# Performance work log

Measured on AMD Instinct MI355X. Metric: run time of the kernel, lower is better.

The kernel has to match this reference:

```python
import jax, jax.numpy as jnp
import numpy as np

N = 100000            # number of nodes
E = 1600000           # number of edges (avg degree 16)
D = 32                # embedding dim
MASK_DEPTH = 3        # cfg.mask_depth
PATH_PROB = 0.5       # cfg.path_prob
NUM_MASK_CAND = 1024  # cfg.num_mask_cand
EPS_NORM = 1e-12      # F.normalize eps


def setup_inputs() -> dict:
    key = jax.random.key(0)
    k1, k2 = jax.random.split(key)
    edge_index = jax.random.randint(k1, (2, E), 0, N)  # [2, E] (row, col) COO indices
    adj_values = jnp.ones((E,), dtype=jnp.float32)     # sparse values (binary adjacency)
    embeds = jax.random.normal(k2, (N, D), dtype=jnp.float32)
    return {"edge_index": edge_index, "adj_values": adj_values, "embeds": embeds}


def _spmm(rows, cols, vals, x):
    # out[i] = sum_{e: rows[e]==i} vals[e] * x[cols[e]]  -- irregular gather + scatter-add
    return jax.ops.segment_sum(x[cols] * vals[:, None], rows, num_segments=N)


def _l2_normalize(x):
    n = jnp.sqrt(jnp.sum(x * x, axis=-1, keepdims=True))
    return x / jnp.maximum(n, EPS_NORM)


def reference(edge_index, adj_values, embeds):
    rows, cols = edge_index[0], edge_index[1]
    vals = adj_values

    # order = row-sums of sparse adj, shape [N, 1]
    order = jax.ops.segment_sum(vals, rows, num_segments=N)[:, None]

    fst_emb = _spmm(rows, cols, vals, embeds) - embeds
    fst_num = order
    emb = [fst_emb]
    num = [fst_num]

    drop_key = jax.random.key(42)
    for i in range(MASK_DEPTH):
        # sparse_dropout with keep prob path_prob**(i+1); zeroing values == dropping edges in spmm
        keep_prob = PATH_PROB ** (i + 1)
        u = jax.random.uniform(jax.random.fold_in(drop_key, i), (E,))
        keep = jnp.floor(u + keep_prob)  # 1.0 with prob keep_prob, else 0.0
        vals = vals * keep               # dropout compounds across iterations

        emb.append(_spmm(rows, cols, vals, emb[-1]) - emb[-1] - order * emb[-1])
        num.append(_spmm(rows, cols, vals, num[-1]) - num[-1] - order)
        order = jax.ops.segment_sum(vals, rows, num_segments=N)[:, None]

    subgraph_embeds = sum(emb) / (sum(num) + 1e-8)
    subgraph_embeds = _l2_normalize(subgraph_embeds)
    embeds_n = _l2_normalize(embeds)

    scores = jnp.sum(subgraph_embeds * embeds_n, axis=-1)  # [N]
    # Gumbel noise: -log(-log(U))
    u = jax.random.uniform(jax.random.key(7), (N,))
    scores = scores + (-jnp.log(-jnp.log(u)))

    _, candidates = jax.lax.top_k(scores, NUM_MASK_CAND)
    return scores, candidates
```

## Files before the change

### kernel.cpp

```cpp
#include <hip/hip_runtime.h>
#include <stdint.h>
#include <stddef.h>

#define NN 100000
#define NE 1600000
#define DD 32
#define NCAND 1024
#define HSIZE 65536
#define SORTN 4096
#define NBUK ((NN + 255) / 256)
#define EPB 4096
#define BCAP 5120
#define BCAPL 4608

#define CAP1 832000
#define CAP2 432000
#define CAP3 240000

__host__ __device__ inline void tf2x32(uint32_t k0, uint32_t k1, uint32_t x0, uint32_t x1,
                                       uint32_t& o0, uint32_t& o1) {
  uint32_t ks2 = k0 ^ k1 ^ 0x1BD11BDAu;
  uint32_t v0 = x0 + k0, v1 = x1 + k1;
#define TFR(r) { v0 += v1; v1 = (v1 << (r)) | (v1 >> (32 - (r))); v1 ^= v0; }
  TFR(13) TFR(15) TFR(26) TFR(6)   v0 += k1;  v1 += ks2 + 1u;
  TFR(17) TFR(29) TFR(16) TFR(24)  v0 += ks2; v1 += k0 + 2u;
  TFR(13) TFR(15) TFR(26) TFR(6)   v0 += k0;  v1 += k1 + 3u;
  TFR(17) TFR(29) TFR(16) TFR(24)  v0 += k1;  v1 += ks2 + 4u;
  TFR(13) TFR(15) TFR(26) TFR(6)   v0 += ks2; v1 += k0 + 5u;
#undef TFR
  o0 = v0; o1 = v1;
}

__device__ __forceinline__ uint32_t jax_bits32(uint32_t k0, uint32_t k1, uint32_t i) {
  uint32_t o0, o1;
  tf2x32(k0, k1, 0u, i, o0, o1);
  return o0 ^ o1;
}

__device__ __forceinline__ float bits_to_uniform(uint32_t b) {
  return __fsub_rn(__uint_as_float((b >> 9) | 0x3f800000u), 1.0f);
}

__device__ __forceinline__ float pairwise32(const float* x) {
  float r[8];
#pragma unroll
  for (int j = 0; j < 8; ++j) r[j] = x[j];
#pragma unroll
  for (int b = 8; b < 32; b += 8)
#pragma unroll
    for (int j = 0; j < 8; ++j) r[j] = __fadd_rn(r[j], x[b + j]);
  float a01 = __fadd_rn(r[0], r[1]), a23 = __fadd_rn(r[2], r[3]);
  float a45 = __fadd_rn(r[4], r[5]), a67 = __fadd_rn(r[6], r[7]);
  return __fadd_rn(__fadd_rn(a01, a23), __fadd_rn(a45, a67));
}


__global__ __launch_bounds__(512) void kA2_bin(
    const int* __restrict__ rows, const int* __restrict__ cols,
    const float* __restrict__ adj,
    uint32_t k00, uint32_t k01, uint32_t k10, uint32_t k11,
    uint32_t k20, uint32_t k21,
    int* __restrict__ bucketCursor, int4* __restrict__ pkBin,
    int* __restrict__ bucketCntS) {
  __shared__ int hist[NBUK];
  __shared__ int base[NBUK];
  __shared__ int h1[NBUK];
  __shared__ int h2[NBUK];
  __shared__ int h3[NBUK];
  __shared__ uint8_t lvs[EPB];
  __shared__ uint16_t rank16[EPB];
  int tid = threadIdx.x;
  for (int i = tid; i < NBUK; i += 512) { hist[i] = 0; h1[i] = 0; h2[i] = 0; h3[i] = 0; }
  __syncthreads();
  int e0 = blockIdx.x * EPB;
  for (int k = 0; k < 8; ++k) {
    int e = e0 + k * 512 + tid;
    int lv = 0;
    if (e < NE) {
      float u0 = bits_to_uniform(jax_bits32(k00, k01, (uint32_t)e));
      float u1 = bits_to_uniform(jax_bits32(k10, k11, (uint32_t)e));
      float u2 = bits_to_uniform(jax_bits32(k20, k21, (uint32_t)e));
      float kp0 = floorf(__fadd_rn(u0, 0.5f));
      float kp1 = floorf(__fadd_rn(u1, 0.25f));
      float kp2 = floorf(__fadd_rn(u2, 0.125f));
      if (kp0 != 0.0f) { lv = 1; if (kp1 != 0.0f) { lv = 2; if (kp2 != 0.0f) lv = 3; } }
      int b = rows[e] >> 8;
      rank16[k * 512 + tid] = (uint16_t)atomicAdd(&hist[b], 1);
      if (lv >= 1) {
        atomicAdd(&h1[b], 1);
        if (lv >= 2) {
          atomicAdd(&h2[b], 1);
          if (lv >= 3) atomicAdd(&h3[b], 1);
        }
      }
    }
    lvs[k * 512 + tid] = (uint8_t)lv;
  }
  __syncthreads();
  for (int i = tid; i < NBUK; i += 512) {
    int h = hist[i];
    base[i] = (h > 0) ? atomicAdd(&bucketCursor[i], h) : 0;
    if (h) atomicAdd(&bucketCntS[i], h);
    if (h1[i]) atomicAdd(&bucketCntS[NBUK + i], h1[i]);
    if (h2[i]) atomicAdd(&bucketCntS[2 * NBUK + i], h2[i]);
    if (h3[i]) atomicAdd(&bucketCntS[3 * NBUK + i], h3[i]);
  }
  __syncthreads();
  for (int k = 0; k < 8; ++k) {
    int e = e0 + k * 512 + tid;
    if (e < NE) {
      int r = rows[e];
      int b = r >> 8;
      int lv = (int)lvs[k * 512 + tid];
      int pos = base[b] + (int)rank16[k * 512 + tid];
      if (pos < BCAP)
        pkBin[(size_t)b * BCAP + pos] =
            make_int4(cols[e], __float_as_int(adj[e]), (e << 2) | lv, r);
    }
  }
}

__global__ __launch_bounds__(512) void k_scanBS(const int* __restrict__ bucketCntS,
                                                int* __restrict__ bucketBaseS) {
  __shared__ int sb[512];
  int a = blockIdx.x;
  const int* c = bucketCntS + (size_t)a * NBUK;
  int* o = bucketBaseS + (size_t)a * (NBUK + 1);
  int tid = threadIdx.x;
  int v = (tid < NBUK) ? c[tid] : 0;
  sb[tid] = v;
  __syncthreads();
  for (int off = 1; off < 512; off <<= 1) {
    int x = (tid >= off) ? sb[tid - off] : 0;
    __syncthreads();
    sb[tid] += x;
    __syncthreads();
  }
  if (tid < NBUK) o[tid] = sb[tid] - v;
  if (tid == NBUK - 1) o[NBUK] = sb[tid];
}

__global__ __launch_bounds__(512) void kB_emit(
    const int* __restrict__ bucketBaseS, const int4* __restrict__ pkBin,
    int* __restrict__ rpAll,
    int2* __restrict__ pk0, int2* __restrict__ pk1,
    int2* __restrict__ pk2, int2* __restrict__ pk3,
    float* __restrict__ order0, float* __restrict__ order1, float* __restrict__ order2) {
  __shared__ unsigned long long cnt64[256];
  __shared__ unsigned long long scan64[512];
  __shared__ int start0[256];
  __shared__ int cur[256];
  __shared__ uint32_t keyF[BCAPL];
  __shared__ uint32_t keyG[BCAPL];
  __shared__ uint16_t origG[BCAPL];
  int b = blockIdx.x, tid = threadIdx.x;
  int bB0 = bucketBaseS[b];
  int n = bucketBaseS[b + 1] - bB0;
  if (n > BCAPL) n = BCAPL;
  size_t sRead = (size_t)b * BCAP;
  const int* pkI = (const int*)pkBin;
  const int2* pkZW = (const int2*)pkBin;
  int r0 = b << 8;
  int nr = NN - r0; if (nr > 256) nr = 256;
  int bB1 = bucketBaseS[(NBUK + 1) + b];
  int bB2 = bucketBaseS[2 * (NBUK + 1) + b];
  int bB3 = bucketBaseS[3 * (NBUK + 1) + b];
  if (tid < 256) { cnt64[tid] = 0ull; cur[tid] = 0; }
  __syncthreads();
  for (int i = tid; i < n; i += 512) {
    int2 zw = pkZW[2 * (sRead + (size_t)i) + 1];
    int lr = zw.y - r0;
    int lv = zw.x & 3;
    keyF[i] = ((uint32_t)lr << 23) | (uint32_t)zw.x;
    unsigned long long add = 1ull;
    if (lv >= 1) add |= 1ull << 16;
    if (lv >= 2) add |= 1ull << 32;
    if (lv >= 3) add |= 1ull << 48;
    atomicAdd(&cnt64[lr], add);
  }
  __syncthreads();
  unsigned long long own = (tid < 256) ? cnt64[tid] : 0ull;
  if (tid < 256) scan64[tid] = own;
  __syncthreads();
  for (int off = 1; off < 256; off <<= 1) {
    unsigned long long v = (tid < 256 && tid >= off) ? scan64[tid - off] : 0ull;
    __syncthreads();
    if (tid < 256) scan64[tid] += v;
    __syncthreads();
  }
  if (tid < 256) {
    unsigned long long ex = scan64[tid] - own;
    start0[tid] = (int)(ex & 0xFFFFull);
    if (tid < nr) {
      rpAll[r0 + tid] = bB0 + (int)(ex & 0xFFFFull);
      rpAll[(NN + 1) + r0 + tid] = bB1 + (int)((ex >> 16) & 0xFFFFull);
      rpAll[2 * (NN + 1) + r0 + tid] = bB2 + (int)((ex >> 32) & 0xFFFFull);
      rpAll[3 * (NN + 1) + r0 + tid] = bB3 + (int)((ex >> 48) & 0xFFFFull);
    }
  }
  if (b == NBUK - 1 && tid == 0) {
    rpAll[NN] = bucketBaseS[NBUK];
    rpAll[(NN + 1) + NN] = bucketBaseS[(NBUK + 1) + NBUK];
    rpAll[2 * (NN + 1) + NN] = bucketBaseS[2 * (NBUK + 1) + NBUK];
    rpAll[3 * (NN + 1) + NN] = bucketBaseS[3 * (NBUK + 1) + NBUK];
  }
  __syncthreads();
  for (int i = tid; i < n; i += 512) {
    uint32_t k = keyF[i];
    int lr = (int)(k >> 23);
    int slot = start0[lr] + atomicAdd(&cur[lr], 1);
    origG[slot] = (uint16_t)i;
    keyG[slot] = k;
  }
  __syncthreads();
  int C2 = (n + 511) >> 9;
  {
    int lo2 = tid * C2, hi2 = lo2 + C2;
    if (lo2 > n) lo2 = n;
    if (hi2 > n) hi2 = n;
    uint16_t vals[10];
    uint16_t pos[10];
    uint32_t keys[10];
#pragma unroll
    for (int q = 0; q < 10; ++q) {
      int i = lo2 + q;
      if (i < hi2) {
        uint32_t ki = keyG[i];
        int lr = (int)(ki >> 23);
        int st = start0[lr];
        int d = (int)(cnt64[lr] & 0xFFFFull);
        int rank = 0;
        for (int j = 0; j < d; ++j) rank += (keyG[st + j] < ki) ? 1 : 0;
        vals[q] = origG[i];
        keys[q] = ki;
        pos[q] = (uint16_t)(st + rank);
      }
    }
    __syncthreads();
#pragma unroll
    for (int q = 0; q < 10; ++q) {
      int i = lo2 + q;
      if (i < hi2) { origG[pos[q]] = vals[q]; keyG[pos[q]] = keys[q]; }
    }
  }
  __syncthreads();
  uint32_t* adjS = keyF;
  {
    uint32_t av[10];
#pragma unroll
    for (int q = 0; q < 10; ++q) {
      int i = tid + q * 512;
      if (i < n) av[q] = (uint32_t)pkI[4 * (sRead + (size_t)origG[i]) + 1];
    }
#pragma unroll
    for (int q = 0; q < 10; ++q) {
      int i = tid + q * 512;
      if (i < n) adjS[i] = av[q];
    }
  }
  __syncthreads();
  if (tid < nr) {
    int d = (int)(cnt64[tid] & 0xFFFFull);
    int st = start0[tid];
    float o0 = 0.0f, o1v = 0.0f, o2v = 0.0f;
    for (int i = 0; i < d; ++i) {
      int lv = (int)(keyG[st + i] & 3u);
      float a = __uint_as_float(adjS[st + i]);
      o0 = __fadd_rn(o0, a);
      if (lv >= 1) { o1v = __fadd_rn(o1v, a); if (lv >= 2) o2v = __fadd_rn(o2v, a); }
    }
    order0[r0 + tid] = o0; order1[r0 + tid] = o1v; order2[r0 + tid] = o2v;
  }
  int lo = tid * C2, hi = lo + C2;
  if (lo > n) lo = n;
  if (hi > n) hi = n;
  int c1 = 0, c2 = 0, c3 = 0;
  for (int i = lo; i < hi; ++i) {
    int lv = (int)(keyG[i] & 3u);
    c1 += (lv >= 1); c2 += (lv >= 2); c3 += (lv >= 3);
  }
  unsigned long long mine = (unsigned long long)c1 |
                            ((unsigned long long)c2 << 16) |
                            ((unsigned long long)c3 << 32);
  ps64_scan:
  scan64[tid] = mine;
  __syncthreads();
  for (int off = 1; off < 512; off <<= 1) {
    unsigned long long v = (tid >= off) ? scan64[tid - off] : 0ull;
    __syncthreads();
    scan64[tid] += v;
    __syncthreads();
  }
  unsigned long long ex = scan64[tid] - mine;
  int o1 = bB1 + (int)(ex & 0xFFFFull);
  int o2 = bB2 + (int)((ex >> 16) & 0xFFFFull);
  int o3 = bB3 + (int)((ex >> 32) & 0xFFFFull);
  {
    int colr[10];
#pragma unroll
    for (int q = 0; q < 10; ++q) {
      int i = lo + q;
      if (i < hi) colr[q] = pkI[4 * (sRead + (size_t)origG[i])];
    }
#pragma unroll
    for (int q = 0; q < 10; ++q) {
      int i = lo + q;
      if (i < hi) {
        int lv = (int)(keyG[i] & 3u);
        int2 pkv = make_int2(colr[q], (int)adjS[i]);
        pk0[bB0 + i] = pkv;
        if (lv >= 1) {
          pk1[o1++] = pkv;
          if (lv >= 2) {
            pk2[o2++] = pkv;
            if (lv >= 3) pk3[o3++] = pkv;
          }
        }
      }
    }
  }
}


__global__ void k_emb0(const int* __restrict__ rp, const int2* __restrict__ pk,
                       const float* __restrict__ embeds, float* __restrict__ e0) {
  int tid = blockIdx.x * blockDim.x + threadIdx.x;
  int r = tid >> 5, d = tid & 31;
  if (r >= NN) return;
  int s = rp[r], t = rp[r + 1];
  float acc = 0.0f;
  for (int base = s; base < t; base += 32) {
    int idx = base + d;
    int2 p = (idx < t) ? pk[idx] : make_int2(0, 0);
    int m = t - base; if (m > 32) m = 32;
    for (int j = 0; j < m; j += 8) {
      int cc[8], aa[8];
      float xx[8];
#pragma unroll
      for (int q = 0; q < 8; ++q) {
        cc[q] = __shfl(p.x, j + q, 32);
        aa[q] = __shfl(p.y, j + q, 32);
      }
#pragma unroll
      for (int q = 0; q < 8; ++q) xx[q] = embeds[(size_t)cc[q] * DD + d];
#pragma unroll
      for (int q = 0; q < 8; ++q)
        acc = __fadd_rn(acc, __fmul_rn(__int_as_float(aa[q]), xx[q]));
    }
  }
  e0[(size_t)r * DD + d] = __fsub_rn(acc, embeds[(size_t)r * DD + d]);
}

__global__ void k_emb_step(const int* __restrict__ rp, const int2* __restrict__ pk,
                           const float* __restrict__ ord, const float* __restrict__ ecur,
                           float* __restrict__ enext, float* __restrict__ esum,
                           const float* __restrict__ ncur, float* __restrict__ nnext,
                           float* __restrict__ nsum, int mode) {
  int tid = blockIdx.x * blockDim.x + threadIdx.x;
  int r = tid >> 5, d = tid & 31;
  if (r >= NN) return;
  int s = rp[r], t = rp[r + 1];
  float acc = 0.0f, accn = 0.0f;
  for (int base = s; base < t; base += 32) {
    int idx = base + d;
    int2 p = (idx < t) ? pk[idx] : make_int2(0, 0);
    int m = t - base; if (m > 32) m = 32;
    for (int j = 0; j < m; j += 8) {
      int cc[8], aa[8];
      float xx[8], nn[8];
#pragma unroll
      for (int q = 0; q < 8; ++q) {
        cc[q] = __shfl(p.x, j + q, 32);
        aa[q] = __shfl(p.y, j + q, 32);
      }
#pragma unroll
      for (int q = 0; q < 8; ++q) {
        xx[q] = ecur[(size_t)cc[q] * DD + d];
        nn[q] = ncur[cc[q]];
      }
#pragma unroll
      for (int q = 0; q < 8; ++q) {
        float av = __int_as_float(aa[q]);
        acc = __fadd_rn(acc, __fmul_rn(av, xx[q]));
        accn = __fadd_rn(accn, __fmul_rn(av, nn[q]));
      }
    }
  }
  float ordv = ord[r];
  size_t idx = (size_t)r * DD + d;
  float ec = ecur[idx];
  float o = __fsub_rn(__fsub_rn(acc, ec), __fmul_rn(ordv, ec));
  if (mode != 3) enext[idx] = o;
  if (mode == 1) esum[idx] = __fadd_rn(ec, o);
  else esum[idx] = __fadd_rn(esum[idx], o);
  if (d == 0) {
    float nc = ncur[r];
    float on = __fsub_rn(__fsub_rn(accn, nc), ordv);
    if (mode != 3) nnext[r] = on;
    if (mode == 1) nsum[r] = __fadd_rn(nc, on);
    else nsum[r] = __fadd_rn(nsum[r], on);
  }
}

__global__ void k_final(const float* __restrict__ embeds, const float* __restrict__ emb_sum,
                        const float* __restrict__ num_sum, uint32_t gk0, uint32_t gk1,
                        float* __restrict__ out_scores, int* __restrict__ hist) {
  int r = blockIdx.x * blockDim.x + threadIdx.x;
  if (r >= NN) return;
  float denom = __fadd_rn(num_sum[r], 1e-8f);
  float sub[DD], em[DD], pr[DD];
  const float4* ps = (const float4*)(emb_sum + (size_t)r * DD);
  const float4* pe = (const float4*)(embeds + (size_t)r * DD);
#pragma unroll
  for (int j = 0; j < 8; ++j) {
    float4 a = ps[j], b = pe[j];
    sub[4 * j + 0] = __fdiv_rn(a.x, denom); sub[4 * j + 1] = __fdiv_rn(a.y, denom);
    sub[4 * j + 2] = __fdiv_rn(a.z, denom); sub[4 * j + 3] = __fdiv_rn(a.w, denom);
    em[4 * j + 0] = b.x; em[4 * j + 1] = b.y; em[4 * j + 2] = b.z; em[4 * j + 3] = b.w;
  }
#pragma unroll
  for (int d = 0; d < DD; ++d) pr[d] = __fmul_rn(sub[d], sub[d]);
  float n1 = fmaxf(__fsqrt_rn(pairwise32(pr)), 1e-12f);
#pragma unroll
  for (int d = 0; d < DD; ++d) pr[d] = __fmul_rn(em[d], em[d]);
  float n2 = fmaxf(__fsqrt_rn(pairwise32(pr)), 1e-12f);
#pragma unroll
  for (int d = 0; d < DD; ++d)
    pr[d] = __fmul_rn(__fdiv_rn(sub[d], n1), __fdiv_rn(em[d], n2));
  float dot = pairwise32(pr);
  float u = bits_to_uniform(jax_bits32(gk0, gk1, (uint32_t)r));
  float l1 = (float)log((double)u);
  float w = -l1;
  float l2 = (float)log((double)w);
  float g = -l2;
  float score = __fadd_rn(dot, g);
  out_scores[r] = score;
  uint32_t kb = __float_as_uint(score);
  kb = (kb & 0x80000000u) ? ~kb : (kb | 0x80000000u);
  atomicAdd(&hist[kb >> 16], 1);
}

__global__ void k_cutoff(const int* __restrict__ hist, int* __restrict__ cutoff) {
  __shared__ int psum[1024];
  int t = threadIdx.x;
  int base = HSIZE - (t + 1) * 64;
  int own = 0;
  for (int i = 0; i < 64; ++i) own += hist[base + i];
  psum[t] = own;
  __syncthreads();
  for (int off = 1; off < 1024; off <<= 1) {
    int v = (t >= off) ? psum[t - off] : 0;
    __syncthreads();
    psum[t] += v;
    __syncthreads();
  }
  int incl = psum[t];
  int prev = incl - own;
  if (incl >= NCAND && prev < NCAND) {
    int c = prev;
    int b = HSIZE - t * 64 - 1;
    while (b >= base) {
      c += hist[b];
      if (c >= NCAND) break;
      --b;
    }
    *cutoff = b;
  }
}

__global__ void k_collect(const float* __restrict__ scores, const int* __restrict__ cutoff,
                          unsigned long long* __restrict__ buf, int* __restrict__ cnt2) {
  int r = blockIdx.x * blockDim.x + threadIdx.x;
  if (r >= NN) return;
  uint32_t kb = __float_as_uint(scores[r]);
  kb = (kb & 0x80000000u) ? ~kb : (kb | 0x80000000u);
  if ((int)(kb >> 16) >= *cutoff) {
    int p = atomicAdd(cnt2, 1);
    if (p < SORTN)
      buf[p] = ((unsigned long long)kb << 32) | (uint32_t)(~(uint32_t)r);
  }
}

__global__ __launch_bounds__(256) void k_rank(const unsigned long long* __restrict__ buf,
                                              const int* __restrict__ cnt2,
                                              float* __restrict__ out_cand) {
  __shared__ unsigned long long s[SORTN];
  int m = *cnt2;
  if (m > SORTN) m = SORTN;
  if (blockIdx.x * 256 >= m) return;
  for (int i = threadIdx.x; i < m; i += 256) s[i] = buf[i];
  __syncthreads();
  int i = blockIdx.x * 256 + threadIdx.x;
  if (i >= m) return;
  unsigned long long mine = s[i];
  int rank = 0;
  int j = 0;
  for (; j + 8 <= m; j += 8) {
#pragma unroll
    for (int q = 0; q < 8; ++q) rank += (s[j + q] > mine) ? 1 : 0;
  }
  for (; j < m; ++j) rank += (s[j] > mine) ? 1 : 0;
  if (rank < NCAND) {
    uint32_t idx = ~((uint32_t)(mine & 0xffffffffull));
    out_cand[rank] = (float)idx;
  }
}

extern "C" void kernel_launch(void* const* d_in, const int* in_sizes, int n_in,
                              void* d_out, int out_size, void* d_ws, size_t ws_size,
                              hipStream_t stream) {
  const int* rows = (const int*)d_in[0];
  const int* cols = rows + NE;
  const float* adj = (const float*)d_in[1];
  const float* embeds = (const float*)d_in[2];
  float* out = (float*)d_out;

  char* p = (char*)d_ws;
  auto alloc = [&](size_t bytes) {
    char* q = p;
    p += (bytes + 255) & ~(size_t)255;
    return q;
  };
  size_t zero_bytes = (size_t)(5 * NBUK + HSIZE + 8) * 4;
  char* zero_base = (char*)alloc(zero_bytes);
  int* bucketCursor = (int*)zero_base;
  int* bucketCntS = bucketCursor + NBUK;
  int* hist = bucketCntS + 4 * NBUK;
  int* cnt2 = hist + HSIZE;

  int* bucketBaseS = (int*)alloc((size_t)4 * (NBUK + 1) * 4);
  int* rpAll = (int*)alloc((size_t)4 * (NN + 1) * 4);
  size_t padBytes = (size_t)NBUK * BCAP * 16;
  char* unionAB = (char*)alloc(padBytes);
  int4* pkBin = (int4*)unionAB;
  float* embA = (float*)unionAB;
  float* embB = (float*)(unionAB + (size_t)NN * DD * 4);
  int2* pk0 = (int2*)alloc((size_t)NE * 8);
  int2* pk1 = (int2*)alloc((size_t)CAP1 * 8);
  int2* pk2 = (int2*)alloc((size_t)CAP2 * 8);
  int2* pk3 = (int2*)alloc((size_t)CAP3 * 8);
  float* embS = (float*)alloc((size_t)NN * DD * 4);
  float* order0 = (float*)alloc(NN * 4);
  float* order1 = (float*)alloc(NN * 4);
  float* order2 = (float*)alloc(NN * 4);
  float* num1 = (float*)alloc(NN * 4);
  float* num2 = (float*)alloc(NN * 4);
  float* numS = (float*)alloc(NN * 4);
  unsigned long long* buf = (unsigned long long*)alloc(SORTN * 8);

  uint32_t dk[3][2];
  for (int i = 0; i < 3; ++i) tf2x32(0u, 42u, 0u, (uint32_t)i, dk[i][0], dk[i][1]);

  hipMemsetAsync(zero_base, 0, zero_bytes, stream);

  int gE = (NE + EPB - 1) / EPB;
  kA2_bin<<<gE, 512, 0, stream>>>(rows, cols, adj, dk[0][0], dk[0][1], dk[1][0], dk[1][1],
                                  dk[2][0], dk[2][1], bucketCursor, pkBin, bucketCntS);
  k_scanBS<<<4, 512, 0, stream>>>(bucketCntS, bucketBaseS);
  kB_emit<<<NBUK, 512, 0, stream>>>(bucketBaseS, pkBin, rpAll,
                                    pk0, pk1, pk2, pk3, order0, order1, order2);

  const int* rp0 = rpAll;
  const int* rp1 = rpAll + (NN + 1);
  const int* rp2 = rpAll + 2 * (NN + 1);
  const int* rp3 = rpAll + 3 * (NN + 1);

  int gEmb = (NN * 32 + 255) / 256;
  k_emb0<<<gEmb, 256, 0, stream>>>(rp0, pk0, embeds, embA);

  k_emb_step<<<gEmb, 256, 0, stream>>>(rp1, pk1, order0, embA, embB, embS,
                                       order0, num1, numS, 1);
  k_emb_step<<<gEmb, 256, 0, stream>>>(rp2, pk2, order1, embB, embA, embS,
                                       num1, num2, numS, 2);
  k_emb_step<<<gEmb, 256, 0, stream>>>(rp3, pk3, order2, embA, embB, embS,
                                       num2, num1, numS, 3);

  k_final<<<(NN + 255) / 256, 256, 0, stream>>>(embeds, embS, numS, 0u, 7u, out, hist);
  k_cutoff<<<1, 1024, 0, stream>>>(hist, cnt2 + 1);
  k_collect<<<(NN + 255) / 256, 256, 0, stream>>>(out, cnt2 + 1, buf, cnt2);
  k_rank<<<(SORTN + 255) / 256, 256, 0, stream>>>(buf, cnt2, out + NN);
}
```

Baseline: 337.0 us.

## Pack per-bucket level counters into one 64-bit shared atomic in binning kernel

The binning kernel now counts all four dropout-level histograms with a single 64-bit shared-memory atomic per edge, using 16-bit fields, instead of up to four separate int atomics. Dropout levels are decided by comparing raw random bits against thresholds rather than converting to floats. Per-edge state is packed into one 32-bit word, so the row is no longer re-read from global memory. The block size is halved to 2048 edges so the rank fits in 11 bits, which doubles the block count and the global atomics on the bucket cursors and counters.

```diff
diff --git a/kernel.cpp b/kernel.cpp
--- a/kernel.cpp
+++ b/kernel.cpp
@@ -9,7 +9,7 @@
 #define HSIZE 65536
 #define SORTN 4096
 #define NBUK ((NN + 255) / 256)
-#define EPB 4096
+#define EPB 2048
 #define BCAP 5120
 #define BCAPL 4608
 
@@ -61,73 +61,70 @@
     uint32_t k00, uint32_t k01, uint32_t k10, uint32_t k11,
     uint32_t k20, uint32_t k21,
     int* __restrict__ bucketCursor, int4* __restrict__ pkBin,
-    int* __restrict__ bucketCntS) {
-  __shared__ int hist[NBUK];
+    unsigned long long* __restrict__ bucketCnt64) {
+  __shared__ unsigned long long cnt64[NBUK];
   __shared__ int base[NBUK];
-  __shared__ int h1[NBUK];
-  __shared__ int h2[NBUK];
-  __shared__ int h3[NBUK];
-  __shared__ uint8_t lvs[EPB];
-  __shared__ uint16_t rank16[EPB];
+  __shared__ uint32_t pack[EPB];
   int tid = threadIdx.x;
-  for (int i = tid; i < NBUK; i += 512) { hist[i] = 0; h1[i] = 0; h2[i] = 0; h3[i] = 0; }
+  for (int i = tid; i < NBUK; i += 512) cnt64[i] = 0ull;
   __syncthreads();
   int e0 = blockIdx.x * EPB;
-  for (int k = 0; k < 8; ++k) {
-    int e = e0 + k * 512 + tid;
-    int lv = 0;
-    if (e < NE) {
-      float u0 = bits_to_uniform(jax_bits32(k00, k01, (uint32_t)e));
-      float u1 = bits_to_uniform(jax_bits32(k10, k11, (uint32_t)e));
-      float u2 = bits_to_uniform(jax_bits32(k20, k21, (uint32_t)e));
-      float kp0 = floorf(__fadd_rn(u0, 0.5f));
-      float kp1 = floorf(__fadd_rn(u1, 0.25f));
-      float kp2 = floorf(__fadd_rn(u2, 0.125f));
-      if (kp0 != 0.0f) { lv = 1; if (kp1 != 0.0f) { lv = 2; if (kp2 != 0.0f) lv = 3; } }
-      int b = rows[e] >> 8;
-      rank16[k * 512 + tid] = (uint16_t)atomicAdd(&hist[b], 1);
-      if (lv >= 1) {
-        atomicAdd(&h1[b], 1);
-        if (lv >= 2) {
-          atomicAdd(&h2[b], 1);
-          if (lv >= 3) atomicAdd(&h3[b], 1);
-        }
-      }
-    }
-    lvs[k * 512 + tid] = (uint8_t)lv;
-  }
-  __syncthreads();
-  for (int i = tid; i < NBUK; i += 512) {
-    int h = hist[i];
-    base[i] = (h > 0) ? atomicAdd(&bucketCursor[i], h) : 0;
-    if (h) atomicAdd(&bucketCntS[i], h);
-    if (h1[i]) atomicAdd(&bucketCntS[NBUK + i], h1[i]);
-    if (h2[i]) atomicAdd(&bucketCntS[2 * NBUK + i], h2[i]);
-    if (h3[i]) atomicAdd(&bucketCntS[3 * NBUK + i], h3[i]);
-  }
-  __syncthreads();
-  for (int k = 0; k < 8; ++k) {
+#pragma unroll
+  for (int k = 0; k < 4; ++k) {
     int e = e0 + k * 512 + tid;
     if (e < NE) {
+      uint32_t b0 = jax_bits32(k00, k01, (uint32_t)e);
+      uint32_t b1 = jax_bits32(k10, k11, (uint32_t)e);
+      uint32_t b2 = jax_bits32(k20, k21, (uint32_t)e);
+      int lv = 0;
+      if (b0 >= 0x80000000u) {
+        lv = 1;
+        if (b1 >= 0xC0000000u) { lv = 2; if (b2 >= 0xE0000000u) lv = 3; }
+      }
       int r = rows[e];
       int b = r >> 8;
-      int lv = (int)lvs[k * 512 + tid];
-      int pos = base[b] + (int)rank16[k * 512 + tid];
+      unsigned long long add = 1ull;
+      if (lv >= 1) add |= 1ull << 16;
+      if (lv >= 2) add |= 1ull << 32;
+      if (lv >= 3) add |= 1ull << 48;
+      unsigned long long old = atomicAdd(&cnt64[b], add);
+      uint32_t rank = (uint32_t)(old & 0xFFFFull);
+      pack[k * 512 + tid] = ((uint32_t)b << 21) | ((uint32_t)(r & 255) << 13) |
+                            ((uint32_t)lv << 11) | rank;
+    }
+  }
+  __syncthreads();
+  for (int i = tid; i < NBUK; i += 512) {
+    unsigned long long h = cnt64[i];
+    int h0 = (int)(h & 0xFFFFull);
+    base[i] = (h0 > 0) ? atomicAdd(&bucketCursor[i], h0) : 0;
+    if (h) atomicAdd(&bucketCnt64[i], h);
+  }
+  __syncthreads();
+#pragma unroll
+  for (int k = 0; k < 4; ++k) {
+    int e = e0 + k * 512 + tid;
+    if (e < NE) {
+      uint32_t pv = pack[k * 512 + tid];
+      int b = (int)(pv >> 21);
+      int lr = (int)((pv >> 13) & 0xFFu);
+      int lv = (int)((pv >> 11) & 3u);
+      int rank = (int)(pv & 0x7FFu);
+      int pos = base[b] + rank;
       if (pos < BCAP)
         pkBin[(size_t)b * BCAP + pos] =
-            make_int4(cols[e], __float_as_int(adj[e]), (e << 2) | lv, r);
-    }
-  }
-}
-
-__global__ __launch_bounds__(512) void k_scanBS(const int* __restrict__ bucketCntS,
+            make_int4(cols[e], __float_as_int(adj[e]), (e << 2) | lv, (b << 8) | lr);
+    }
+  }
+}
+
+__global__ __launch_bounds__(512) void k_scanBS(const unsigned long long* __restrict__ bucketCnt64,
                                                 int* __restrict__ bucketBaseS) {
   __shared__ int sb[512];
   int a = blockIdx.x;
-  const int* c = bucketCntS + (size_t)a * NBUK;
   int* o = bucketBaseS + (size_t)a * (NBUK + 1);
   int tid = threadIdx.x;
-  int v = (tid < NBUK) ? c[tid] : 0;
+  int v = (tid < NBUK) ? (int)((bucketCnt64[tid] >> (16 * a)) & 0xFFFFull) : 0;
   sb[tid] = v;
   __syncthreads();
   for (int off = 1; off < 512; off <<= 1) {
@@ -282,7 +279,6 @@
   unsigned long long mine = (unsigned long long)c1 |
                             ((unsigned long long)c2 << 16) |
                             ((unsigned long long)c3 << 32);
-  ps64_scan:
   scan64[tid] = mine;
   __syncthreads();
   for (int off = 1; off < 512; off <<= 1) {
@@ -521,11 +517,11 @@
     p += (bytes + 255) & ~(size_t)255;
     return q;
   };
-  size_t zero_bytes = (size_t)(5 * NBUK + HSIZE + 8) * 4;
+  size_t zero_bytes = (size_t)(392 + 2 * NBUK + HSIZE + 8) * 4;
   char* zero_base = (char*)alloc(zero_bytes);
   int* bucketCursor = (int*)zero_base;
-  int* bucketCntS = bucketCursor + NBUK;
-  int* hist = bucketCntS + 4 * NBUK;
+  unsigned long long* bucketCnt64 = (unsigned long long*)(zero_base + 392 * 4);
+  int* hist = (int*)(zero_base + (392 + 2 * NBUK) * 4);
   int* cnt2 = hist + HSIZE;
 
   int* bucketBaseS = (int*)alloc((size_t)4 * (NBUK + 1) * 4);
@@ -555,8 +551,8 @@
 
   int gE = (NE + EPB - 1) / EPB;
   kA2_bin<<<gE, 512, 0, stream>>>(rows, cols, adj, dk[0][0], dk[0][1], dk[1][0], dk[1][1],
-                                  dk[2][0], dk[2][1], bucketCursor, pkBin, bucketCntS);
-  k_scanBS<<<4, 512, 0, stream>>>(bucketCntS, bucketBaseS);
+                                  dk[2][0], dk[2][1], bucketCursor, pkBin, bucketCnt64);
+  k_scanBS<<<4, 512, 0, stream>>>(bucketCnt64, bucketBaseS);
   kB_emit<<<NBUK, 512, 0, stream>>>(bucketBaseS, pkBin, rpAll,
                                     pk0, pk1, pk2, pk3, order0, order1, order2);
 
```

Result: slower. 351.8 us (+4.4%).
